# Kernel tuning notes

Hardware: AMD Instinct MI355X
Metric: run time of the kernel (lower is better)

## Reference

```python
import jax, jax.numpy as jnp
import numpy as np

IN_DIM = 128
OUT_DIM = 128
NUM_HEADS = 4
HEAD_DIM = OUT_DIM // NUM_HEADS
NEG_SLOPE = 0.2


def setup_inputs() -> dict:
    key = jax.random.key(0)
    k1, k2, k3, k4, k5 = jax.random.split(key, 5)
    B, N = 8, 1024
    x = jax.random.normal(k1, (B, N, IN_DIM), dtype=jnp.float32)
    alive = jax.random.uniform(k2, (B, N), dtype=jnp.float32)  # ~half alive (>=0.5)
    # nn.Linear(in_dim, H*D, bias=False): weight shape [H*D, in_dim]
    W = jax.random.normal(k3, (NUM_HEADS * HEAD_DIM, IN_DIM), dtype=jnp.float32) / np.sqrt(IN_DIM)
    a_src = jax.random.normal(k4, (NUM_HEADS, HEAD_DIM), dtype=jnp.float32) / np.sqrt(HEAD_DIM)
    a_dst = jax.random.normal(k5, (NUM_HEADS, HEAD_DIM), dtype=jnp.float32) / np.sqrt(HEAD_DIM)
    return {"x": x, "alive": alive, "W": W, "a_src": a_src, "a_dst": a_dst}


def reference(x, alive, W, a_src, a_dst):
    B, N, _ = x.shape
    # h: [B, N, H, D]
    h = (x @ W.T).reshape(B, N, NUM_HEADS, HEAD_DIM)
    alpha_src = jnp.einsum('bnhd,hd->bnh', h, a_src)  # [B, N, H]
    alpha_dst = jnp.einsum('bnhd,hd->bnh', h, a_dst)  # [B, N, H]
    # e[b, i(query), j(key), h]
    e = alpha_src[:, :, None, :] + alpha_dst[:, None, :, :]
    e = jnp.where(e >= 0, e, NEG_SLOPE * e)  # LeakyReLU(0.2)
    key_mask = alive[:, None, :, None] >= 0.5  # [B, 1, N, 1] over key axis
    e = jnp.where(key_mask, e, -jnp.inf)
    attn = jax.nn.softmax(e, axis=2)
    attn = jnp.nan_to_num(attn, nan=0.0)
    out = jnp.einsum('bqkh,bkhd->bqhd', attn, h)  # weighted sum over keys
    return out.reshape(B, N, NUM_HEADS * HEAD_DIM)
```

## Files before the change

### kernel.cpp

```cpp
#include <hip/hip_runtime.h>
#include <hip/hip_bf16.h>


#define B_   8
#define N_   1024
#define BN   (B_ * N_)
#define IND  128
#define H_   4
#define D_   32
#define NEG  0.2f
#define CH   16
#define NCH  (N_ / CH)
#define QB   64

typedef float float4_ __attribute__((ext_vector_type(4)));
typedef short short8_ __attribute__((ext_vector_type(8)));

__device__ __forceinline__ float bf2f(ushort u) {
    union { unsigned int i; float f; } v; v.i = ((unsigned int)u) << 16; return v.f;
}
__device__ __forceinline__ ushort f2bf(float f) {
    union { float f; unsigned int i; } v; v.f = f;
    unsigned int lsb = (v.i >> 16) & 1u;
    v.i += 0x7fffu + lsb;
    return (ushort)(v.i >> 16);
}
__device__ __forceinline__ unsigned int orderable(float f) {
    unsigned int u = __float_as_uint(f);
    return (u & 0x80000000u) ? ~u : (u | 0x80000000u);
}
__device__ __forceinline__ short8_ pack_hi(float4_ a, float4_ b) {
    short8_ r;
    r[0] = (short)f2bf(a[0]); r[1] = (short)f2bf(a[1]);
    r[2] = (short)f2bf(a[2]); r[3] = (short)f2bf(a[3]);
    r[4] = (short)f2bf(b[0]); r[5] = (short)f2bf(b[1]);
    r[6] = (short)f2bf(b[2]); r[7] = (short)f2bf(b[3]);
    return r;
}
__device__ __forceinline__ void split_bf(float4_ a, float4_ b, short8_& hi, short8_& lo) {
    #pragma unroll
    for (int j = 0; j < 4; ++j) {
        ushort h0 = f2bf(a[j]); hi[j]     = (short)h0; lo[j]     = (short)f2bf(a[j] - bf2f(h0));
        ushort h1 = f2bf(b[j]); hi[j + 4] = (short)h1; lo[j + 4] = (short)f2bf(b[j] - bf2f(h1));
    }
}

__global__ __launch_bounds__(256) void k_gemm_alpha(
    const float* __restrict__ x,
    const float* __restrict__ alive,
    const float* __restrict__ W,
    const float* __restrict__ a_src,
    const float* __restrict__ a_dst,
    float* __restrict__ h_ws,
    float* __restrict__ sT,
    float* __restrict__ tT,
    float* __restrict__ e1T,
    float* __restrict__ e2T)
{
    __shared__ float hs[32][132];
    __shared__ float asrc[IND], adst[IND];

    const int tid = threadIdx.x;
    const int wv  = tid >> 6;
    const int ln  = tid & 63;
    const int l15 = ln & 15;
    const int lg  = ln >> 4;
    const int rbase = blockIdx.x * 32;

    if (tid < IND) { asrc[tid] = a_src[tid]; adst[tid] = a_dst[tid]; }

    short8_ bf[2][4];
    #pragma unroll
    for (int t = 0; t < 2; ++t) {
        const float* wr = &W[(size_t)((wv * 2 + t) * 16 + l15) * IND + lg * 8];
        #pragma unroll
        for (int ks = 0; ks < 4; ++ks) {
            float4_ v0 = *reinterpret_cast<const float4_*>(wr + ks * 32);
            float4_ v1 = *reinterpret_cast<const float4_*>(wr + ks * 32 + 4);
            bf[t][ks] = pack_hi(v0, v1);
        }
    }

    float4_ acc[2][2];
    #pragma unroll
    for (int mt = 0; mt < 2; ++mt) {
        const float* xr = &x[(size_t)(rbase + mt * 16 + l15) * IND + lg * 8];
        short8_ ahi[4], alo[4];
        #pragma unroll
        for (int ks = 0; ks < 4; ++ks) {
            float4_ v0 = *reinterpret_cast<const float4_*>(xr + ks * 32);
            float4_ v1 = *reinterpret_cast<const float4_*>(xr + ks * 32 + 4);
            split_bf(v0, v1, ahi[ks], alo[ks]);
        }
        #pragma unroll
        for (int t = 0; t < 2; ++t) {
            float4_ a = {0.f, 0.f, 0.f, 0.f};
            #pragma unroll
            for (int ks = 0; ks < 4; ++ks) {
                a = __builtin_amdgcn_mfma_f32_16x16x32_bf16(ahi[ks], bf[t][ks], a, 0, 0, 0);
                a = __builtin_amdgcn_mfma_f32_16x16x32_bf16(alo[ks], bf[t][ks], a, 0, 0, 0);
            }
            acc[mt][t] = a;
        }
    }

    #pragma unroll
    for (int mt = 0; mt < 2; ++mt)
        #pragma unroll
        for (int t = 0; t < 2; ++t) {
            const int col = (wv * 2 + t) * 16 + l15;
            #pragma unroll
            for (int r = 0; r < 4; ++r)
                hs[mt * 16 + lg * 4 + r][col] = acc[mt][t][r];
        }
    __syncthreads();

    #pragma unroll
    for (int i = tid; i < 1024; i += 256) {
        int row = i >> 5, c4 = (i & 31) * 4;
        *reinterpret_cast<float4_*>(&h_ws[(size_t)(rbase + row) * IND + c4]) =
            *reinterpret_cast<const float4_*>(&hs[row][c4]);
    }

    if (tid < 128) {
        const int row = tid >> 2, hh = tid & 3;
        const float* hr = &hs[row][hh * 32];
        float s = 0.f, tt = 0.f;
        #pragma unroll
        for (int d = 0; d < 32; ++d) {
            s  = fmaf(hr[d], asrc[hh * 32 + d], s);
            tt = fmaf(hr[d], adst[hh * 32 + d], tt);
        }
        const int grow = rbase + row;
        const int idx  = hh * BN + grow;
        sT[idx] = s;
        tT[idx] = tt;
        float am = (alive[grow] >= 0.5f) ? 1.f : 0.f;
        e1T[idx] = am * __expf(tt);
        e2T[idx] = am * __expf(NEG * tt);
    }
}

__global__ __launch_bounds__(256) void k_rank(
    const float* __restrict__ tT,
    const float* __restrict__ e1T,
    const float* __restrict__ e2T,
    float* __restrict__ tSg,
    int*   __restrict__ kIg,
    float* __restrict__ e1g,
    float* __restrict__ e2g)
{
    __shared__ unsigned long long keys[N_];
    __shared__ int part[128];
    const int h = blockIdx.y, b = blockIdx.z;
    const int base = h * BN + b * N_;
    for (int i = threadIdx.x; i < N_; i += 256) {
        unsigned int u = orderable(tT[base + i]);
        keys[i] = ((unsigned long long)u << 32) | (unsigned int)i;
    }
    __syncthreads();

    const int own  = threadIdx.x & 127;
    const int half = threadIdx.x >> 7;
    const int i0   = blockIdx.x * 128 + own;
    const unsigned long long mk = keys[i0];
    int rank = 0;
    const ulonglong2* k2p = reinterpret_cast<const ulonglong2*>(keys) + half * 256;
    #pragma unroll 8
    for (int j = 0; j < 256; ++j) {
        ulonglong2 kk = k2p[j];
        rank += (int)(kk.x < mk) + (int)(kk.y < mk);
    }
    if (half) part[own] = rank;
    __syncthreads();
    if (!half) {
        rank += part[own];
        const int o = (b * H_ + h) * N_ + rank;
        tSg[o] = tT[base + i0];
        kIg[o] = i0;
        e1g[o] = e1T[base + i0];
        e2g[o] = e2T[base + i0];
    }
}

__global__ __launch_bounds__(512) void k_comb(
    const float* __restrict__ h_ws,
    const float* __restrict__ sT,
    const float* __restrict__ tSg,
    const int*   __restrict__ kIg,
    const float* __restrict__ e1g,
    const float* __restrict__ e2g,
    float* __restrict__ out)
{
    __shared__ float tS[N_];
    __shared__ int   kI[N_];
    __shared__ float e1S[N_], e2S[N_];
    __shared__ float pre2[NCH + 1][36];
    __shared__ float suf1[NCH + 2][36];
    __shared__ float dpre2[NCH + 1], dsuf1[NCH + 2];

    const int h = blockIdx.y, b = blockIdx.z, qb = blockIdx.x;
    const int bhi = b * H_ + h;
    const int so  = bhi * N_;
    const int tid = threadIdx.x;

    for (int i = tid; i < N_; i += 512) {
        tS[i]  = tSg[so + i];
        kI[i]  = kIg[so + i];
        e1S[i] = e1g[so + i];
        e2S[i] = e2g[so + i];
    }
    __syncthreads();

    {
        const int cc = tid >> 3, dg = tid & 7;
        float4_ a1 = {0.f, 0.f, 0.f, 0.f}, a2 = {0.f, 0.f, 0.f, 0.f};
        #pragma unroll
        for (int jj = 0; jj < CH; ++jj) {
            const int j = cc * CH + jj;
            const float4_ hv = *reinterpret_cast<const float4_*>(
                &h_ws[(size_t)(b * N_ + kI[j]) * IND + h * D_ + dg * 4]);
            a1 += e1S[j] * hv;
            a2 += e2S[j] * hv;
        }
        #pragma unroll
        for (int u = 0; u < 4; ++u) {
            pre2[cc + 1][dg * 4 + u] = a2[u];
            suf1[cc][dg * 4 + u]     = a1[u];
        }
        if (tid < NCH) {
            float s2 = 0.f;
            #pragma unroll
            for (int jj = 0; jj < CH; ++jj) s2 += e2S[tid * CH + jj];
            dpre2[tid + 1] = s2;
        } else if (tid < 2 * NCH) {
            const int c2 = tid - NCH;
            float s1 = 0.f;
            #pragma unroll
            for (int jj = 0; jj < CH; ++jj) s1 += e1S[c2 * CH + jj];
            dsuf1[c2] = s1;
        }
    }
    __syncthreads();

    {
        const int wv = tid >> 6, lane = tid & 63;
        if (wv < 4) {
            for (int d = wv; d < D_; d += 4) {
                float v = pre2[lane + 1][d];
                #pragma unroll
                for (int off = 1; off < 64; off <<= 1) {
                    float n = __shfl_up(v, off);
                    if (lane >= off) v += n;
                }
                pre2[lane + 1][d] = v;
                if (lane == 0) pre2[0][d] = 0.f;
            }
            if (wv == 0) {
                float v = dpre2[lane + 1];
                #pragma unroll
                for (int off = 1; off < 64; off <<= 1) {
                    float n = __shfl_up(v, off);
                    if (lane >= off) v += n;
                }
                dpre2[lane + 1] = v;
                if (lane == 0) dpre2[0] = 0.f;
            }
        } else {
            for (int d = wv - 4; d < D_; d += 4) {
                float v = suf1[lane][d];
                #pragma unroll
                for (int off = 1; off < 64; off <<= 1) {
                    float n = __shfl_down(v, off);
                    if (lane < 64 - off) v += n;
                }
                suf1[lane][d] = v;
                if (lane == 0) { suf1[NCH][d] = 0.f; suf1[NCH + 1][d] = 0.f; }
            }
            if (wv == 4) {
                float v = dsuf1[lane];
                #pragma unroll
                for (int off = 1; off < 64; off <<= 1) {
                    float n = __shfl_down(v, off);
                    if (lane < 64 - off) v += n;
                }
                dsuf1[lane] = v;
                if (lane == 0) { dsuf1[NCH] = 0.f; dsuf1[NCH + 1] = 0.f; }
            }
        }
    }
    __syncthreads();

    const int ql  = tid >> 3;
    const int sub = tid & 7;
    const int ln  = tid & 63;
    const int q   = qb * QB + ql;

    const float s  = sT[h * BN + b * N_ + q];
    const float A  = __expf(s);
    const float Bv = __expf(NEG * s);

    int p = 0;
    if (sub == 0) {
        const float tau = -s;
        int lo = 0, hi = N_;
        #pragma unroll
        for (int it = 0; it < 10; ++it) {
            int mid = (lo + hi) >> 1;
            if (tS[mid] >= tau) hi = mid; else lo = mid + 1;
        }
        p = lo;
    }
    p = __shfl(p, ln & 56);
    const int cp = p >> 4;

    float4_ acc = A  * (*reinterpret_cast<const float4_*>(&suf1[cp + 1][sub * 4]))
                + Bv * (*reinterpret_cast<const float4_*>(&pre2[cp][sub * 4]));
    float den = A * dsuf1[cp + 1] + Bv * dpre2[cp];
    if (cp < NCH) {
        #pragma unroll
        for (int jj = 0; jj < CH; ++jj) {
            const int j = (cp << 4) + jj;
            const float w = (j < p) ? Bv * e2S[j] : A * e1S[j];
            const float4_ hv = *reinterpret_cast<const float4_*>(
                &h_ws[(size_t)(b * N_ + kI[j]) * IND + h * D_ + sub * 4]);
            acc += w * hv;
            den += w;
        }
    }

    const float inv = (den > 0.f) ? 1.f / den : 0.f;
    float4_ r = acc * inv;
    *reinterpret_cast<float4_*>(&out[(size_t)(b * N_ + q) * IND + h * D_ + sub * 4]) = r;
}

extern "C" void kernel_launch(void* const* d_in, const int* in_sizes, int n_in,
                              void* d_out, int out_size, void* d_ws, size_t ws_size,
                              hipStream_t stream) {
    const float* x     = (const float*)d_in[0];
    const float* alive = (const float*)d_in[1];
    const float* W     = (const float*)d_in[2];
    const float* a_src = (const float*)d_in[3];
    const float* a_dst = (const float*)d_in[4];
    float* out = (float*)d_out;

    float* h_ws   = (float*)d_ws;
    float* sT     = h_ws + (size_t)BN * IND;
    float* tT     = sT  + (size_t)H_ * BN;
    float* e1T    = tT  + (size_t)H_ * BN;
    float* e2T    = e1T + (size_t)H_ * BN;
    float* tSg    = e2T + (size_t)H_ * BN;
    int*   kIg    = (int*)(tSg + 32 * N_);
    float* e1g    = (float*)(kIg + 32 * N_);
    float* e2g    = e1g + 32 * N_;

    k_gemm_alpha<<<BN / 32, 256, 0, stream>>>(x, alive, W, a_src, a_dst,
                                              h_ws, sT, tT, e1T, e2T);

    dim3 g2(N_ / 128, H_, B_);
    k_rank<<<g2, 256, 0, stream>>>(tT, e1T, e2T, tSg, kIg, e1g, e2g);

    dim3 g4(N_ / QB, H_, B_);
    k_comb<<<g4, 512, 0, stream>>>(h_ws, sT, tSg, kIg, e1g, e2g, out);
}
```

Measured before the change: 37.39 us.

## Scatter h rows into sorted order in rank kernel and pack per-key scalars

The rank kernel now writes each key's h head-slice (32 floats) to a buffer laid out in sorted order, and packs the t, e1 and e2 values into one float4 per key. The combine kernel then reads h contiguously by sorted index instead of gathering through the kI indirection, and loads the per-key scalars with one vector load. This removes the indirect, scattered global reads in the hot combine loops. In exchange the rank kernel does extra global writes, a full copy of h in permuted order per head.

Result: slower. 38.56 us (median of 2 runs) (+3.1%).

```diff
diff --git a/kernel.cpp b/kernel.cpp
--- a/kernel.cpp
+++ b/kernel.cpp
@@ -145,13 +145,12 @@
     const float* __restrict__ tT,
     const float* __restrict__ e1T,
     const float* __restrict__ e2T,
-    float* __restrict__ tSg,
-    int*   __restrict__ kIg,
-    float* __restrict__ e1g,
-    float* __restrict__ e2g)
+    const float* __restrict__ h_ws,
+    float4_* __restrict__ packed,
+    float* __restrict__ hg)
 {
     __shared__ unsigned long long keys[N_];
-    __shared__ int part[128];
+    __shared__ int part[2][128];
     const int h = blockIdx.y, b = blockIdx.z;
     const int base = h * BN + b * N_;
     for (int i = threadIdx.x; i < N_; i += 256) {
@@ -171,29 +170,33 @@
         ulonglong2 kk = k2p[j];
         rank += (int)(kk.x < mk) + (int)(kk.y < mk);
     }
-    if (half) part[own] = rank;
-    __syncthreads();
+    part[half][own] = rank;
+    __syncthreads();
+    rank += part[1 - half][own];
+
+    const int o = (b * H_ + h) * N_ + rank;
     if (!half) {
-        rank += part[own];
-        const int o = (b * H_ + h) * N_ + rank;
-        tSg[o] = tT[base + i0];
-        kIg[o] = i0;
-        e1g[o] = e1T[base + i0];
-        e2g[o] = e2T[base + i0];
-    }
+        float4_ pk;
+        pk[0] = tT[base + i0];
+        pk[1] = e1T[base + i0];
+        pk[2] = e2T[base + i0];
+        pk[3] = 0.f;
+        packed[o] = pk;
+    }
+    const float4_* src = reinterpret_cast<const float4_*>(
+        &h_ws[(size_t)(b * N_ + i0) * IND + h * D_ + half * 16]);
+    float4_* dst = reinterpret_cast<float4_*>(&hg[(size_t)o * D_ + half * 16]);
+    #pragma unroll
+    for (int u = 0; u < 4; ++u) dst[u] = src[u];
 }
 
 __global__ __launch_bounds__(512) void k_comb(
-    const float* __restrict__ h_ws,
+    const float* __restrict__ hg,
     const float* __restrict__ sT,
-    const float* __restrict__ tSg,
-    const int*   __restrict__ kIg,
-    const float* __restrict__ e1g,
-    const float* __restrict__ e2g,
+    const float4_* __restrict__ packed,
     float* __restrict__ out)
 {
     __shared__ float tS[N_];
-    __shared__ int   kI[N_];
     __shared__ float e1S[N_], e2S[N_];
     __shared__ float pre2[NCH + 1][36];
     __shared__ float suf1[NCH + 2][36];
@@ -205,10 +208,10 @@
     const int tid = threadIdx.x;
 
     for (int i = tid; i < N_; i += 512) {
-        tS[i]  = tSg[so + i];
-        kI[i]  = kIg[so + i];
-        e1S[i] = e1g[so + i];
-        e2S[i] = e2g[so + i];
+        const float4_ pk = packed[so + i];
+        tS[i]  = pk[0];
+        e1S[i] = pk[1];
+        e2S[i] = pk[2];
     }
     __syncthreads();
 
@@ -219,7 +222,7 @@
         for (int jj = 0; jj < CH; ++jj) {
             const int j = cc * CH + jj;
             const float4_ hv = *reinterpret_cast<const float4_*>(
-                &h_ws[(size_t)(b * N_ + kI[j]) * IND + h * D_ + dg * 4]);
+                &hg[(size_t)(so + j) * D_ + dg * 4]);
             a1 += e1S[j] * hv;
             a2 += e2S[j] * hv;
         }
@@ -323,7 +326,7 @@
             const int j = (cp << 4) + jj;
             const float w = (j < p) ? Bv * e2S[j] : A * e1S[j];
             const float4_ hv = *reinterpret_cast<const float4_*>(
-                &h_ws[(size_t)(b * N_ + kI[j]) * IND + h * D_ + sub * 4]);
+                &hg[(size_t)(so + j) * D_ + sub * 4]);
             acc += w * hv;
             den += w;
         }
@@ -344,22 +347,20 @@
     const float* a_dst = (const float*)d_in[4];
     float* out = (float*)d_out;
 
-    float* h_ws   = (float*)d_ws;
-    float* sT     = h_ws + (size_t)BN * IND;
-    float* tT     = sT  + (size_t)H_ * BN;
-    float* e1T    = tT  + (size_t)H_ * BN;
-    float* e2T    = e1T + (size_t)H_ * BN;
-    float* tSg    = e2T + (size_t)H_ * BN;
-    int*   kIg    = (int*)(tSg + 32 * N_);
-    float* e1g    = (float*)(kIg + 32 * N_);
-    float* e2g    = e1g + 32 * N_;
+    float*   h_ws   = (float*)d_ws;
+    float*   sT     = h_ws + (size_t)BN * IND;
+    float*   tT     = sT  + (size_t)H_ * BN;
+    float*   e1T    = tT  + (size_t)H_ * BN;
+    float*   e2T    = e1T + (size_t)H_ * BN;
+    float4_* packed = (float4_*)(e2T + (size_t)H_ * BN);
+    float*   hg     = (float*)(packed + 32 * N_);
 
     k_gemm_alpha<<<BN / 32, 256, 0, stream>>>(x, alive, W, a_src, a_dst,
                                               h_ws, sT, tT, e1T, e2T);
 
     dim3 g2(N_ / 128, H_, B_);
-    k_rank<<<g2, 256, 0, stream>>>(tT, e1T, e2T, tSg, kIg, e1g, e2g);
+    k_rank<<<g2, 256, 0, stream>>>(tT, e1T, e2T, h_ws, packed, hg);
 
     dim3 g4(N_ / QB, H_, B_);
-    k_comb<<<g4, 512, 0, stream>>>(h_ws, sT, tSg, kIg, e1g, e2g, out);
-}
+    k_comb<<<g4, 512, 0, stream>>>(hg, sT, packed, out);
+}
```
